# Performance work log

Measured on AMD Instinct MI355X. Metric: run time of the kernel, lower is better.

The kernel has to match this reference:

```python
import jax, jax.numpy as jnp
import numpy as np

IN_DIM = 768
HID = 128
NUM_CLASSES = 32
N_NODES = 50000
N_EDGES = 1600000


def setup_inputs() -> dict:
    key = jax.random.key(0)
    ks = jax.random.split(key, 8)
    x = jax.random.normal(ks[0], (N_NODES, IN_DIM), dtype=jnp.float32)
    edge_index = jax.random.randint(ks[1], (2, N_EDGES), 0, N_NODES, dtype=jnp.int64)
    # GCNConv weights (PyG: linear without bias inside propagate, bias added after aggregation)
    W1 = jax.random.normal(ks[2], (IN_DIM, HID), dtype=jnp.float32) / np.sqrt(IN_DIM)
    b1 = jnp.zeros((HID,), dtype=jnp.float32)
    W2 = jax.random.normal(ks[3], (HID, HID), dtype=jnp.float32) / np.sqrt(HID)
    b2 = jnp.zeros((HID,), dtype=jnp.float32)
    Wfc = jax.random.normal(ks[4], (HID, NUM_CLASSES), dtype=jnp.float32) / np.sqrt(HID)
    bfc = jnp.zeros((NUM_CLASSES,), dtype=jnp.float32)
    return {"x": x, "edge_index": edge_index, "W1": W1, "b1": b1,
            "W2": W2, "b2": b2, "Wfc": Wfc, "bfc": bfc}


def _gcn_conv(x, src, dst, norm, W, b, num_nodes):
    # PyG GCNConv: h = x @ W; out[i] = sum_j norm_ij * h[j]; out += b
    h = x @ W                      # [N, out_dim]
    msgs = h[src] * norm[:, None]  # gather + scale, [E+N, out_dim]
    out = jax.ops.segment_sum(msgs, dst, num_segments=num_nodes)
    return out + b


def reference(x, edge_index, W1, b1, W2, b2, Wfc, bfc):
    n = x.shape[0]
    loop = jnp.arange(n, dtype=edge_index.dtype)
    src = jnp.concatenate([edge_index[0], loop])  # add self-loops
    dst = jnp.concatenate([edge_index[1], loop])
    # symmetric normalization: deg computed on destination with unit edge weights
    deg = jax.ops.segment_sum(jnp.ones_like(src, dtype=x.dtype), dst, num_segments=n)
    dinv = jnp.where(deg > 0, jax.lax.rsqrt(jnp.maximum(deg, 1.0)), 0.0)
    norm = dinv[src] * dinv[dst]  # [E+N]

    h = jax.nn.relu(_gcn_conv(x, src, dst, norm, W1, b1, n))
    h = jax.nn.relu(_gcn_conv(h, src, dst, norm, W2, b2, n))
    return h @ Wfc + bfc
```

## Files before the change

kernel.cpp:

```cpp
#include <hip/hip_runtime.h>
#include <hip/hip_bf16.h>
#include <hip/hip_fp16.h>

#define N_NODES 50000
#define IN_DIM 768
#define HID 128
#define NCLS 32
#define CHUNK 8192
#define NBUCK ((N_NODES + 255) >> 8)

typedef __attribute__((ext_vector_type(8))) short bf16x8;
typedef __attribute__((ext_vector_type(4))) float f32x4;
typedef __attribute__((ext_vector_type(4))) unsigned short u16x4;

__device__ inline void split_bf16(float x, unsigned short& hi, unsigned short& lo) {
    unsigned int u = __float_as_uint(x);
    hi = (unsigned short)(u >> 16);
    float r = x - __uint_as_float(u & 0xFFFF0000u);
    lo = (unsigned short)(__float_as_uint(r) >> 16);
}

__global__ __launch_bounds__(256) void count_bucket(const int* __restrict__ raw, int E,
                                                    int* __restrict__ hist) {
    __shared__ int cnt[NBUCK];
    bool is64 = (raw[1] == 0 && raw[3] == 0 && raw[5] == 0 && raw[7] == 0);
    int t = threadIdx.x, b = blockIdx.x;
    if (t < NBUCK) cnt[t] = 0;
    __syncthreads();
    int base = b * CHUNK;
#pragma unroll
    for (int j = 0; j < CHUNK / 256; ++j) {
        int e = base + j * 256 + t;
        if (e < E) {
            int d = is64 ? raw[2 * (E + e)] : raw[E + e];
            atomicAdd(&cnt[d >> 8], 1);
        }
    }
    __syncthreads();
    if (t < NBUCK) hist[b * NBUCK + t] = cnt[t];
}

__global__ __launch_bounds__(256) void scan_off2(const int* __restrict__ hist, int nblk,
                                                 int E, int* __restrict__ bstart,
                                                 int* __restrict__ off) {
    __shared__ int tot[256];
    int t = threadIdx.x;
    int sum = 0;
    if (t < NBUCK)
        for (int b = 0; b < nblk; ++b) sum += hist[b * NBUCK + t];
    tot[t] = (t < NBUCK) ? sum : 0;
    __syncthreads();
    for (int o = 1; o < 256; o <<= 1) {
        int v = (t >= o) ? tot[t - o] : 0;
        __syncthreads();
        tot[t] += v;
        __syncthreads();
    }
    int excl = (t == 0) ? 0 : tot[t - 1];
    if (t < NBUCK) {
        bstart[t] = excl;
        int run = excl;
        for (int b = 0; b < nblk; ++b) {
            off[b * NBUCK + t] = run;
            run += hist[b * NBUCK + t];
        }
    }
    if (t == 0) bstart[NBUCK] = E;
}

__global__ __launch_bounds__(256) void chunk_scatter(const int* __restrict__ raw, int E,
                                                     const int* __restrict__ off,
                                                     unsigned int* __restrict__ ebuf) {
    __shared__ int offl[NBUCK];
    __shared__ int cnt[NBUCK];
    bool is64 = (raw[1] == 0 && raw[3] == 0 && raw[5] == 0 && raw[7] == 0);
    int t = threadIdx.x, b = blockIdx.x;
    if (t < NBUCK) { offl[t] = off[b * NBUCK + t]; cnt[t] = 0; }
    __syncthreads();
    int base = b * CHUNK;
#pragma unroll
    for (int j = 0; j < CHUNK / 256; ++j) {
        int e = base + j * 256 + t;
        if (e < E) {
            int s, d;
            if (is64) { s = raw[2 * e]; d = raw[2 * (E + e)]; }
            else      { s = raw[e];     d = raw[E + e]; }
            int k = d >> 8;
            int r = atomicAdd(&cnt[k], 1);
            ebuf[offl[k] + r] = ((unsigned int)(d & 255) << 16) | (unsigned int)s;
        }
    }
}

__global__ __launch_bounds__(256) void bucket_fine2(const unsigned int* __restrict__ ebuf,
                                                    const int* __restrict__ bstart,
                                                    int* __restrict__ rowp,
                                                    float* __restrict__ dinv,
                                                    unsigned short* __restrict__ csr,
                                                    int n, int E) {
    __shared__ int cnt[256];
    __shared__ int pre[256];
    __shared__ int fil[256];
    int k = blockIdx.x, t = threadIdx.x;
    int base = k << 8;
    int nn = min(256, n - base);
    int es = bstart[k], ee = bstart[k + 1];
    cnt[t] = 0;
    __syncthreads();
    for (int p = es + t; p < ee; p += 256) atomicAdd(&cnt[ebuf[p] >> 16], 1);
    __syncthreads();
    pre[t] = cnt[t];
    __syncthreads();
    for (int o = 1; o < 256; o <<= 1) {
        int v = (t >= o) ? pre[t - o] : 0;
        __syncthreads();
        pre[t] += v;
        __syncthreads();
    }
    int excl = (t == 0) ? 0 : pre[t - 1];
    if (t < nn) {
        rowp[base + t] = es + excl;
        dinv[base + t] = rsqrtf((float)(cnt[t] + 1));
    }
    if (k == gridDim.x - 1 && t == 0) rowp[n] = E;
    fil[t] = es + excl;
    __syncthreads();
    for (int p = es + t; p < ee; p += 256) {
        unsigned int u = ebuf[p];
        int q = atomicAdd(&fil[u >> 16], 1);
        csr[q] = (unsigned short)(u & 0xFFFFu);
    }
}

__global__ void pack_w(const float* __restrict__ W, int K,
                       unsigned short* __restrict__ ph, unsigned short* __restrict__ pl) {
    int gid = blockIdx.x * 256 + threadIdx.x;
    int total = (K / 32) * 8 * 64;
    if (gid >= total) return;
    int l = gid & 63;
    int c0 = (gid >> 6) & 7;
    int t = gid >> 9;
    int col = c0 * 16 + (l & 15);
    int k0 = t * 32 + ((l >> 4) << 3);
    size_t base = (size_t)gid * 8;
#pragma unroll
    for (int j = 0; j < 8; ++j) {
        unsigned short h, lo;
        split_bf16(W[(size_t)(k0 + j) * 128 + col], h, lo);
        ph[base + j] = h;
        pl[base + j] = lo;
    }
}

template <bool AHALF>
__device__ inline float4 loadA4(const void* A, size_t idx) {
    if constexpr (AHALF) {
        uint2 u = *(const uint2*)((const __half*)A + idx);
        float2 f0 = __half22float2(*(__half2*)&u.x);
        float2 f1 = __half22float2(*(__half2*)&u.y);
        return make_float4(f0.x, f0.y, f1.x, f1.y);
    } else {
        return *(const float4*)((const float*)A + idx);
    }
}

template <int K, bool AHALF>
__global__ __launch_bounds__(256) void gemm_mfma4(const void* __restrict__ A,
                                                  const unsigned short* __restrict__ Bph,
                                                  const unsigned short* __restrict__ Bpl,
                                                  const float* __restrict__ dinv,
                                                  __half* __restrict__ Chalf, int M) {
    __shared__ unsigned short Ah[2][64][72];
    __shared__ unsigned short Al[2][64][72];
    int tid = threadIdx.x;
    int wid = tid >> 6, lane = tid & 63;
    int wr = wid >> 1, wc = wid & 1;
    int row0 = blockIdx.x * 64;
    int lrow = lane & 15;
    const int T = K / 64;

    int sr[4], sc[4];
    bool vv[4];
    size_t abase[4];
#pragma unroll
    for (int q = 0; q < 4; ++q) {
        int idx = q * 256 + tid;
        sr[q] = idx >> 4;
        sc[q] = (idx & 15) * 4;
        vv[q] = (row0 + sr[q]) < M;
        abase[q] = (size_t)(row0 + sr[q]) * K + sc[q];
    }

    float4 pre[4];
#pragma unroll
    for (int q = 0; q < 4; ++q)
        pre[q] = vv[q] ? loadA4<AHALF>(A, abase[q]) : make_float4(0.f, 0.f, 0.f, 0.f);

#pragma unroll
    for (int q = 0; q < 4; ++q) {
        u16x4 h, lo;
        split_bf16(pre[q].x, ((unsigned short*)&h)[0], ((unsigned short*)&lo)[0]);
        split_bf16(pre[q].y, ((unsigned short*)&h)[1], ((unsigned short*)&lo)[1]);
        split_bf16(pre[q].z, ((unsigned short*)&h)[2], ((unsigned short*)&lo)[2]);
        split_bf16(pre[q].w, ((unsigned short*)&h)[3], ((unsigned short*)&lo)[3]);
        *(u16x4*)&Ah[0][sr[q]][sc[q]] = h;
        *(u16x4*)&Al[0][sr[q]][sc[q]] = lo;
    }
    __syncthreads();

    f32x4 acc[2][4] = {};
    int cur = 0;
    for (int t = 0; t < T; ++t) {
        if (t + 1 < T) {
#pragma unroll
            for (int q = 0; q < 4; ++q)
                pre[q] = vv[q] ? loadA4<AHALF>(A, abase[q] + (size_t)(t + 1) * 64)
                               : make_float4(0.f, 0.f, 0.f, 0.f);
        }
#pragma unroll
        for (int ks = 0; ks < 2; ++ks) {
            int lk2 = ks * 32 + (lane >> 4) * 8;
            bf16x8 ah[2], al[2];
#pragma unroll
            for (int m = 0; m < 2; ++m) {
                int r = wr * 32 + m * 16 + lrow;
                ah[m] = *(const bf16x8*)&Ah[cur][r][lk2];
                al[m] = *(const bf16x8*)&Al[cur][r][lk2];
            }
            int t32 = t * 2 + ks;
            bf16x8 bh[4], bl[4];
#pragma unroll
            for (int n = 0; n < 4; ++n) {
                size_t boff = ((size_t)(t32 * 8 + wc * 4 + n) * 64 + lane) * 8;
                bh[n] = *(const bf16x8*)&Bph[boff];
                bl[n] = *(const bf16x8*)&Bpl[boff];
            }
#pragma unroll
            for (int m = 0; m < 2; ++m)
#pragma unroll
                for (int n = 0; n < 4; ++n) {
                    acc[m][n] = __builtin_amdgcn_mfma_f32_16x16x32_bf16(ah[m], bh[n], acc[m][n], 0, 0, 0);
                    acc[m][n] = __builtin_amdgcn_mfma_f32_16x16x32_bf16(al[m], bh[n], acc[m][n], 0, 0, 0);
                    acc[m][n] = __builtin_amdgcn_mfma_f32_16x16x32_bf16(ah[m], bl[n], acc[m][n], 0, 0, 0);
                }
        }
        if (t + 1 < T) {
            int nxt = cur ^ 1;
#pragma unroll
            for (int q = 0; q < 4; ++q) {
                u16x4 h, lo;
                split_bf16(pre[q].x, ((unsigned short*)&h)[0], ((unsigned short*)&lo)[0]);
                split_bf16(pre[q].y, ((unsigned short*)&h)[1], ((unsigned short*)&lo)[1]);
                split_bf16(pre[q].z, ((unsigned short*)&h)[2], ((unsigned short*)&lo)[2]);
                split_bf16(pre[q].w, ((unsigned short*)&h)[3], ((unsigned short*)&lo)[3]);
                *(u16x4*)&Ah[nxt][sr[q]][sc[q]] = h;
                *(u16x4*)&Al[nxt][sr[q]][sc[q]] = lo;
            }
            __syncthreads();
            cur = nxt;
        }
    }
#pragma unroll
    for (int m = 0; m < 2; ++m) {
        int rbase = row0 + wr * 32 + m * 16 + (lane >> 4) * 4;
#pragma unroll
        for (int n = 0; n < 4; ++n) {
            int col = wc * 64 + n * 16 + lrow;
#pragma unroll
            for (int j = 0; j < 4; ++j) {
                int r = rbase + j;
                if (r < M) Chalf[(size_t)r * 128 + col] = __float2half(dinv[r] * acc[m][n][j]);
            }
        }
    }
}

__global__ __launch_bounds__(256) void aggregate5(const __half* __restrict__ ht,
                                                  const int* __restrict__ rowp,
                                                  const unsigned short* __restrict__ csr,
                                                  const float* __restrict__ dinv,
                                                  const float* __restrict__ bias,
                                                  __half* __restrict__ outh, int n) {
    int wid = threadIdx.x >> 6, lane = threadIdx.x & 63;
    int i = blockIdx.x * 4 + wid;
    if (i >= n) return;
    const __half2* h2 = (const __half2*)ht;
    float di = dinv[i];
    float2 acc = __half22float2(h2[(size_t)i * 64 + lane]);
    int b = rowp[i], e = rowp[i + 1];
    int p = b;
    for (; p + 16 <= e; p += 16) {
        int s[16]; float2 v[16];
#pragma unroll
        for (int q = 0; q < 16; ++q) s[q] = csr[p + q];
#pragma unroll
        for (int q = 0; q < 16; ++q) v[q] = __half22float2(h2[(size_t)s[q] * 64 + lane]);
#pragma unroll
        for (int q = 0; q < 16; ++q) { acc.x += v[q].x; acc.y += v[q].y; }
    }
    for (; p + 4 <= e; p += 4) {
        int s[4]; float2 v[4];
#pragma unroll
        for (int q = 0; q < 4; ++q) s[q] = csr[p + q];
#pragma unroll
        for (int q = 0; q < 4; ++q) v[q] = __half22float2(h2[(size_t)s[q] * 64 + lane]);
#pragma unroll
        for (int q = 0; q < 4; ++q) { acc.x += v[q].x; acc.y += v[q].y; }
    }
    for (; p < e; ++p) {
        float2 v = __half22float2(h2[(size_t)csr[p] * 64 + lane]);
        acc.x += v.x;
        acc.y += v.y;
    }
    float2 bb = ((const float2*)bias)[lane];
    __half2 o = __floats2half2_rn(fmaxf(di * acc.x + bb.x, 0.f),
                                  fmaxf(di * acc.y + bb.y, 0.f));
    ((__half2*)outh)[(size_t)i * 64 + lane] = o;
}

__global__ __launch_bounds__(256) void fc_out(const __half* __restrict__ h,
                                              const float* __restrict__ W,
                                              const float* __restrict__ b,
                                              float* __restrict__ out, int n) {
    __shared__ float Ws[HID * NCLS];
    __shared__ float Hs[8][HID];
    int tid = threadIdx.x;
#pragma unroll
    for (int l = 0; l < 16; ++l) Ws[l * 256 + tid] = W[l * 256 + tid];
    int row0 = blockIdx.x * 8;
#pragma unroll
    for (int l = 0; l < 4; ++l) {
        int idx = l * 256 + tid;
        int r = idx >> 7, c = idx & 127;
        int gr = row0 + r;
        Hs[r][c] = (gr < n) ? __half2float(h[(size_t)gr * HID + c]) : 0.f;
    }
    __syncthreads();
    int r = tid >> 5, c = tid & 31;
    float acc = b[c];
#pragma unroll
    for (int k = 0; k < HID; ++k) acc += Hs[r][k] * Ws[k * NCLS + c];
    int gr = row0 + r;
    if (gr < n) out[(size_t)gr * NCLS + c] = acc;
}

extern "C" void kernel_launch(void* const* d_in, const int* in_sizes, int n_in,
                              void* d_out, int out_size, void* d_ws, size_t ws_size,
                              hipStream_t stream) {
    const float* x   = (const float*)d_in[0];
    const int*   eid = (const int*)d_in[1];
    const float* W1  = (const float*)d_in[2];
    const float* b1  = (const float*)d_in[3];
    const float* W2  = (const float*)d_in[4];
    const float* b2  = (const float*)d_in[5];
    const float* Wfc = (const float*)d_in[6];
    const float* bfc = (const float*)d_in[7];
    float* out = (float*)d_out;

    const int N = N_NODES;
    const int E = in_sizes[1] / 2;
    const int NBLK = (E + CHUNK - 1) / CHUNK;

    auto align = [](size_t v) { return (v + 255) & ~(size_t)255; };
    char* w = (char*)d_ws;
    size_t off = 0;
    int* rowp = (int*)(w + off);           off = align(off + (size_t)(N + 1) * 4);
    float* dinv = (float*)(w + off);       off = align(off + (size_t)N * 4);
    unsigned short* csr = (unsigned short*)(w + off); off = align(off + (size_t)E * 2);
    unsigned int* ebuf = (unsigned int*)(w + off);    off = align(off + (size_t)E * 4);
    int* bstart = (int*)(w + off);         off = align(off + (size_t)(NBUCK + 1) * 4);
    int* hist = (int*)(w + off);           off = align(off + (size_t)NBLK * NBUCK * 4);
    int* offs = (int*)(w + off);           off = align(off + (size_t)NBLK * NBUCK * 4);
    unsigned short* W1ph = (unsigned short*)(w + off); off = align(off + (size_t)128 * IN_DIM * 2);
    unsigned short* W1pl = (unsigned short*)(w + off); off = align(off + (size_t)128 * IN_DIM * 2);
    unsigned short* W2ph = (unsigned short*)(w + off); off = align(off + (size_t)128 * HID * 2);
    unsigned short* W2pl = (unsigned short*)(w + off); off = align(off + (size_t)128 * HID * 2);
    __half* ht1 = (__half*)(w + off);      off = align(off + (size_t)N * HID * 2);
    __half* ht2 = (__half*)(w + off);      off = align(off + (size_t)N * HID * 2);
    __half* h1r = (__half*)(w + off);      off = align(off + (size_t)N * HID * 2);
    __half* h2r = (__half*)(w + off);      off = align(off + (size_t)N * HID * 2);

    count_bucket<<<NBLK, 256, 0, stream>>>(eid, E, hist);
    scan_off2<<<1, 256, 0, stream>>>(hist, NBLK, E, bstart, offs);
    chunk_scatter<<<NBLK, 256, 0, stream>>>(eid, E, offs, ebuf);
    bucket_fine2<<<NBUCK, 256, 0, stream>>>(ebuf, bstart, rowp, dinv, csr, N, E);

    pack_w<<<((IN_DIM / 32) * 8 * 64 + 255) / 256, 256, 0, stream>>>(W1, IN_DIM, W1ph, W1pl);
    pack_w<<<((HID / 32) * 8 * 64 + 255) / 256, 256, 0, stream>>>(W2, HID, W2ph, W2pl);

    int gb = (N + 63) / 64;
    int ab = (N + 3) / 4;
    gemm_mfma4<IN_DIM, false><<<gb, 256, 0, stream>>>(x, W1ph, W1pl, dinv, ht1, N);
    aggregate5<<<ab, 256, 0, stream>>>(ht1, rowp, csr, dinv, b1, h1r, N);
    gemm_mfma4<HID, true><<<gb, 256, 0, stream>>>(h1r, W2ph, W2pl, dinv, ht2, N);
    aggregate5<<<ab, 256, 0, stream>>>(ht2, rowp, csr, dinv, b2, h2r, N);
    fc_out<<<(N + 7) / 8, 256, 0, stream>>>(h2r, Wfc, bfc, out, N);
}
```

Before: 300.7 us.

## Restructure GEMM to single-buffered LDS with templated K-tile and register prefetch

```diff
diff --git a/kernel.cpp b/kernel.cpp
--- a/kernel.cpp
+++ b/kernel.cpp
@@ -18,6 +18,13 @@
     hi = (unsigned short)(u >> 16);
     float r = x - __uint_as_float(u & 0xFFFF0000u);
     lo = (unsigned short)(__float_as_uint(r) >> 16);
+}
+
+__device__ inline void split4(const float4& v, u16x4& h, u16x4& lo) {
+    split_bf16(v.x, ((unsigned short*)&h)[0], ((unsigned short*)&lo)[0]);
+    split_bf16(v.y, ((unsigned short*)&h)[1], ((unsigned short*)&lo)[1]);
+    split_bf16(v.z, ((unsigned short*)&h)[2], ((unsigned short*)&lo)[2]);
+    split_bf16(v.w, ((unsigned short*)&h)[3], ((unsigned short*)&lo)[3]);
 }
 
 __global__ __launch_bounds__(256) void count_bucket(const int* __restrict__ raw, int E,
@@ -164,76 +171,72 @@
     }
 }
 
-template <int K, bool AHALF>
-__global__ __launch_bounds__(256) void gemm_mfma4(const void* __restrict__ A,
+template <int K, int BKT, bool AHALF>
+__global__ __launch_bounds__(256) void gemm_mfma8(const void* __restrict__ A,
                                                   const unsigned short* __restrict__ Bph,
                                                   const unsigned short* __restrict__ Bpl,
                                                   const float* __restrict__ dinv,
                                                   __half* __restrict__ Chalf, int M) {
-    __shared__ unsigned short Ah[2][64][72];
-    __shared__ unsigned short Al[2][64][72];
+    constexpr int QPR = BKT / 4;
+    constexpr int NQ = 64 * QPR / 256;
+    constexpr int NSUB = BKT / 32;
+    __shared__ unsigned short Ah[64][BKT + 8];
+    __shared__ unsigned short Al[64][BKT + 8];
     int tid = threadIdx.x;
     int wid = tid >> 6, lane = tid & 63;
     int wr = wid >> 1, wc = wid & 1;
     int row0 = blockIdx.x * 64;
     int lrow = lane & 15;
-    const int T = K / 64;
-
-    int sr[4], sc[4];
-    bool vv[4];
-    size_t abase[4];
-#pragma unroll
-    for (int q = 0; q < 4; ++q) {
+    const int T = K / BKT;
+
+    int sr[NQ], sc[NQ];
+    bool vv[NQ];
+    size_t ai[NQ];
+#pragma unroll
+    for (int q = 0; q < NQ; ++q) {
         int idx = q * 256 + tid;
-        sr[q] = idx >> 4;
-        sc[q] = (idx & 15) * 4;
+        sr[q] = idx / QPR;
+        sc[q] = (idx % QPR) * 4;
         vv[q] = (row0 + sr[q]) < M;
-        abase[q] = (size_t)(row0 + sr[q]) * K + sc[q];
-    }
-
-    float4 pre[4];
-#pragma unroll
-    for (int q = 0; q < 4; ++q)
-        pre[q] = vv[q] ? loadA4<AHALF>(A, abase[q]) : make_float4(0.f, 0.f, 0.f, 0.f);
-
-#pragma unroll
-    for (int q = 0; q < 4; ++q) {
-        u16x4 h, lo;
-        split_bf16(pre[q].x, ((unsigned short*)&h)[0], ((unsigned short*)&lo)[0]);
-        split_bf16(pre[q].y, ((unsigned short*)&h)[1], ((unsigned short*)&lo)[1]);
-        split_bf16(pre[q].z, ((unsigned short*)&h)[2], ((unsigned short*)&lo)[2]);
-        split_bf16(pre[q].w, ((unsigned short*)&h)[3], ((unsigned short*)&lo)[3]);
-        *(u16x4*)&Ah[0][sr[q]][sc[q]] = h;
-        *(u16x4*)&Al[0][sr[q]][sc[q]] = lo;
-    }
-    __syncthreads();
+        ai[q] = (size_t)(row0 + sr[q]) * K + sc[q];
+    }
+
+    float4 z = make_float4(0.f, 0.f, 0.f, 0.f);
+    float4 pre[NQ];
+#pragma unroll
+    for (int q = 0; q < NQ; ++q) pre[q] = vv[q] ? loadA4<AHALF>(A, ai[q]) : z;
 
     f32x4 acc[2][4] = {};
-    int cur = 0;
     for (int t = 0; t < T; ++t) {
-        if (t + 1 < T) {
-#pragma unroll
-            for (int q = 0; q < 4; ++q)
-                pre[q] = vv[q] ? loadA4<AHALF>(A, abase[q] + (size_t)(t + 1) * 64)
-                               : make_float4(0.f, 0.f, 0.f, 0.f);
-        }
-#pragma unroll
-        for (int ks = 0; ks < 2; ++ks) {
+#pragma unroll
+        for (int q = 0; q < NQ; ++q) {
+            u16x4 h, lo;
+            split4(pre[q], h, lo);
+            *(u16x4*)&Ah[sr[q]][sc[q]] = h;
+            *(u16x4*)&Al[sr[q]][sc[q]] = lo;
+        }
+        __syncthreads();
+#pragma unroll
+        for (int ks = 0; ks < NSUB; ++ks) {
             int lk2 = ks * 32 + (lane >> 4) * 8;
+            bf16x8 bh[4], bl[4];
+#pragma unroll
+            for (int n = 0; n < 4; ++n) {
+                size_t boff = ((size_t)((t * NSUB + ks) * 8 + wc * 4 + n) * 64 + lane) * 8;
+                bh[n] = *(const bf16x8*)&Bph[boff];
+                bl[n] = *(const bf16x8*)&Bpl[boff];
+            }
+            if (ks == 0 && t + 1 < T) {
+#pragma unroll
+                for (int q = 0; q < NQ; ++q)
+                    pre[q] = vv[q] ? loadA4<AHALF>(A, ai[q] + (size_t)(t + 1) * BKT) : z;
+            }
             bf16x8 ah[2], al[2];
 #pragma unroll
             for (int m = 0; m < 2; ++m) {
                 int r = wr * 32 + m * 16 + lrow;
-                ah[m] = *(const bf16x8*)&Ah[cur][r][lk2];
-                al[m] = *(const bf16x8*)&Al[cur][r][lk2];
-            }
-            int t32 = t * 2 + ks;
-            bf16x8 bh[4], bl[4];
-#pragma unroll
-            for (int n = 0; n < 4; ++n) {
-                size_t boff = ((size_t)(t32 * 8 + wc * 4 + n) * 64 + lane) * 8;
-                bh[n] = *(const bf16x8*)&Bph[boff];
-                bl[n] = *(const bf16x8*)&Bpl[boff];
+                ah[m] = *(const bf16x8*)&Ah[r][lk2];
+                al[m] = *(const bf16x8*)&Al[r][lk2];
             }
 #pragma unroll
             for (int m = 0; m < 2; ++m)
@@ -244,21 +247,7 @@
                     acc[m][n] = __builtin_amdgcn_mfma_f32_16x16x32_bf16(ah[m], bl[n], acc[m][n], 0, 0, 0);
                 }
         }
-        if (t + 1 < T) {
-            int nxt = cur ^ 1;
-#pragma unroll
-            for (int q = 0; q < 4; ++q) {
-                u16x4 h, lo;
-                split_bf16(pre[q].x, ((unsigned short*)&h)[0], ((unsigned short*)&lo)[0]);
-                split_bf16(pre[q].y, ((unsigned short*)&h)[1], ((unsigned short*)&lo)[1]);
-                split_bf16(pre[q].z, ((unsigned short*)&h)[2], ((unsigned short*)&lo)[2]);
-                split_bf16(pre[q].w, ((unsigned short*)&h)[3], ((unsigned short*)&lo)[3]);
-                *(u16x4*)&Ah[nxt][sr[q]][sc[q]] = h;
-                *(u16x4*)&Al[nxt][sr[q]][sc[q]] = lo;
-            }
-            __syncthreads();
-            cur = nxt;
-        }
+        __syncthreads();
     }
 #pragma unroll
     for (int m = 0; m < 2; ++m) {
@@ -390,9 +379,9 @@
 
     int gb = (N + 63) / 64;
     int ab = (N + 3) / 4;
-    gemm_mfma4<IN_DIM, false><<<gb, 256, 0, stream>>>(x, W1ph, W1pl, dinv, ht1, N);
+    gemm_mfma8<IN_DIM, 96, false><<<gb, 256, 0, stream>>>(x, W1ph, W1pl, dinv, ht1, N);
     aggregate5<<<ab, 256, 0, stream>>>(ht1, rowp, csr, dinv, b1, h1r, N);
-    gemm_mfma4<HID, true><<<gb, 256, 0, stream>>>(h1r, W2ph, W2pl, dinv, ht2, N);
+    gemm_mfma8<HID, 32, true><<<gb, 256, 0, stream>>>(h1r, W2ph, W2pl, dinv, ht2, N);
     aggregate5<<<ab, 256, 0, stream>>>(ht2, rowp, csr, dinv, b2, h2r, N);
     fc_out<<<(N + 7) / 8, 256, 0, stream>>>(h2r, Wfc, bfc, out, N);
 }
```

Result: no change. 295.2 us (-1.8%).
